# Kernel tuning notes

Measured on AMD Instinct MI355X. Metric: run time of the kernel, lower is better.

## Reference

```python
import jax, jax.numpy as jnp
import numpy as np

N_NODES = 50000


def _degree_norm(src, dst, n):
    # symmetric GCN normalization with self-loops already appended
    deg = jax.ops.segment_sum(jnp.ones(src.shape[0], jnp.float32), dst, num_segments=n)
    dinv = jnp.where(deg > 0, jax.lax.rsqrt(deg), 0.0)
    return dinv[src] * dinv[dst]  # [E_full]


def _gcn_layer(x, W, b, src, dst, norm, n):
    h = x @ W                                  # [N, out]
    msgs = h[src] * norm[:, None]              # gather + scale, [E_full, out]
    out = jax.ops.segment_sum(msgs, dst, num_segments=n)
    return out + b


def setup_inputs() -> dict:
    key = jax.random.key(0)
    k1, k2, k3, k4 = jax.random.split(key, 4)
    n, e, d_in, d_out = N_NODES, 800000, 256, 128
    x = jax.random.normal(k1, (n, d_in), jnp.float32)
    edge_index = jax.random.randint(k2, (2, e), 0, n, dtype=jnp.int64)
    W1 = jax.random.normal(k3, (d_in, 2 * d_out), jnp.float32) / np.sqrt(d_in)
    b1 = jnp.zeros((2 * d_out,), jnp.float32)
    W2 = jax.random.normal(k4, (2 * d_out, d_out), jnp.float32) / np.sqrt(2 * d_out)
    b2 = jnp.zeros((d_out,), jnp.float32)
    return {"x": x, "edge_index": edge_index, "W1": W1, "b1": b1, "W2": W2, "b2": b2}


def reference(x, edge_index, W1, b1, W2, b2):
    n = x.shape[0]
    loops = jnp.arange(n, dtype=edge_index.dtype)
    src = jnp.concatenate([edge_index[0], loops])
    dst = jnp.concatenate([edge_index[1], loops])
    norm = _degree_norm(src, dst, n)
    h = jax.nn.relu(_gcn_layer(x, W1, b1, src, dst, norm, n))
    h = jax.nn.relu(_gcn_layer(h, W2, b2, src, dst, norm, n))
    return h
```

## Files before the change

### kernel.cpp

```cpp
#include <hip/hip_runtime.h>
#include <hip/hip_bf16.h>


typedef __attribute__((ext_vector_type(8))) short bf16x8;
typedef __attribute__((ext_vector_type(8))) unsigned short u16x8;
typedef __attribute__((ext_vector_type(4))) float f32x4;

__device__ inline float bf2f(unsigned short u) {
    return __uint_as_float(((unsigned)u) << 16);
}
__device__ inline unsigned short f2bf(float f) {
    unsigned x = __float_as_uint(f);
    unsigned r = (x + 0x7fffu + ((x >> 16) & 1u)) >> 16;
    return (unsigned short)r;
}

__global__ void degree_kernel(const int* __restrict__ dst, unsigned* __restrict__ deg, int E) {
    int e = blockIdx.x * blockDim.x + threadIdx.x;
    if (e < E) atomicAdd(&deg[dst[e]], 1u);
}

__global__ void dinv_kernel(const unsigned* __restrict__ deg, float* __restrict__ dinv, int N) {
    int i = blockIdx.x * blockDim.x + threadIdx.x;
    if (i < N) dinv[i] = rsqrtf((float)(deg[i] + 1u));
}

#define NBIN 512

__global__ __launch_bounds__(256) void hist_lds_kernel(const unsigned* __restrict__ deg,
                                                       int* __restrict__ hist, int N) {
    __shared__ int lh[NBIN];
    const int t = threadIdx.x;
#pragma unroll
    for (int i = 0; i < NBIN / 256; i++) lh[t + i * 256] = 0;
    __syncthreads();
    int idx = blockIdx.x * 256 + t;
    if (idx < N) {
        int b = (int)deg[idx]; if (b > NBIN - 1) b = NBIN - 1;
        atomicAdd(&lh[NBIN - 1 - b], 1);
    }
    __syncthreads();
#pragma unroll
    for (int i = 0; i < NBIN / 256; i++) {
        int v = lh[t + i * 256];
        if (v) atomicAdd(&hist[t + i * 256], v);
    }
}

__global__ void scan_bins_kernel(const int* __restrict__ hist,
                                 int* __restrict__ binstart,
                                 int* __restrict__ bincur,
                                 int* __restrict__ edgebase,
                                 int* __restrict__ rowptr, int N) {
    const int t = threadIdx.x;
    int cn = 0, ce = 0;
    for (int b = 0; b < NBIN; b += 64) {
        int i = b + t;
        int cnt = hist[i];
        int d = NBIN - 1 - i;
        int d8 = (d + 7) & ~7;
        int en = cnt * d8;
        int xn = cnt, xe = en;
#pragma unroll
        for (int off = 1; off < 64; off <<= 1) {
            int yn = __shfl_up(xn, off, 64);
            int ye = __shfl_up(xe, off, 64);
            if (t >= off) { xn += yn; xe += ye; }
        }
        binstart[i] = cn + xn - cnt;
        bincur[i]   = cn + xn - cnt;
        edgebase[i] = ce + xe - en;
        cn += __shfl(xn, 63, 64);
        ce += __shfl(xe, 63, 64);
    }
    if (t == 0) rowptr[N] = ce;
}

__global__ __launch_bounds__(256) void place_fused_kernel(
    const unsigned* __restrict__ deg,
    int* __restrict__ bincur,
    const int* __restrict__ binstart,
    const int* __restrict__ edgebase,
    int* __restrict__ perm, int* __restrict__ rankv,
    int* __restrict__ rowptr, int* __restrict__ cursor,
    unsigned short* __restrict__ col, int N) {
    __shared__ int lh[NBIN];
    __shared__ int base[NBIN];
    const int t = threadIdx.x;
#pragma unroll
    for (int i = 0; i < NBIN / 256; i++) lh[t + i * 256] = 0;
    __syncthreads();
    int idx = blockIdx.x * 256 + t;
    int bin = 0, lrank = 0;
    if (idx < N) {
        int b = (int)deg[idx]; if (b > NBIN - 1) b = NBIN - 1;
        bin = NBIN - 1 - b;
        lrank = atomicAdd(&lh[bin], 1);
    }
    __syncthreads();
#pragma unroll
    for (int i = 0; i < NBIN / 256; i++) {
        int v = lh[t + i * 256];
        if (v) base[t + i * 256] = atomicAdd(&bincur[t + i * 256], v);
    }
    __syncthreads();
    if (idx < N) {
        int pos = base[bin] + lrank;
        int d = NBIN - 1 - bin;
        int d8 = (d + 7) & ~7;
        int rp = edgebase[bin] + (pos - binstart[bin]) * d8;
        perm[pos] = idx;
        rankv[idx] = pos;
        rowptr[pos] = rp;
        cursor[pos] = rp;
        for (int k = d; k < d8; k++) col[rp + k] = (unsigned short)N;
    }
}

__global__ __launch_bounds__(256) void fill_kernel(const int* __restrict__ src,
                                                   const int* __restrict__ dst,
                                                   const int* __restrict__ rank,
                                                   int* __restrict__ cursor,
                                                   unsigned short* __restrict__ col, int E) {
    int e = blockIdx.x * blockDim.x + threadIdx.x;
    if (e < E) {
        int d = dst[e];
        int pos = atomicAdd(&cursor[rank[d]], 1);
        col[pos] = (unsigned short)src[e];
    }
}

__global__ __launch_bounds__(256) void convert_x_kernel(const float* __restrict__ in,
                                                        const float* __restrict__ dinv,
                                                        unsigned short* __restrict__ out,
                                                        long n4, int ld4) {
    long i = (long)blockIdx.x * blockDim.x + threadIdx.x;
    if (i < n4) {
        float ds = dinv[i / ld4];
        float4 v = ((const float4*)in)[i];
        ushort4 o;
        o.x = f2bf(v.x * ds); o.y = f2bf(v.y * ds);
        o.z = f2bf(v.z * ds); o.w = f2bf(v.w * ds);
        ((ushort4*)out)[i] = o;
    }
}

__global__ __launch_bounds__(256) void convert_wt_kernel(const float* __restrict__ W,
                                                         unsigned short* __restrict__ WT,
                                                         int K, int Nw) {
    int id = blockIdx.x * blockDim.x + threadIdx.x;
    if (id < K * Nw) {
        int k = id / Nw;
        int n = id % Nw;
        WT[(long)n * K + k] = f2bf(W[id]);
    }
}

__global__ void zero_pad_kernel(unsigned short* __restrict__ h1,
                                unsigned short* __restrict__ h2, int Np1) {
    int t = threadIdx.x;
    if (t < 8 * 32) {
        int c = t >> 5, f = t & 31;
        h1[((size_t)c * Np1 + (Np1 - 1)) * 32 + f] = 0;
    } else if (t < 12 * 32) {
        int q = t - 256;
        int c = q >> 5, f = q & 31;
        h2[((size_t)c * Np1 + (Np1 - 1)) * 32 + f] = 0;
    }
}

#define GBM 128
#define GBN 128
#define GBK 64
template <int CH>
__global__ __launch_bounds__(256) void gemm_bf16(const unsigned short* __restrict__ A,
                                                 const unsigned short* __restrict__ BT,
                                                 unsigned short* __restrict__ C,
                                                 int M, int Nc, int K, int ldm) {
    __shared__ __align__(16) unsigned short As[GBM * GBK];
    __shared__ __align__(16) unsigned short Bs[GBN * GBK];
    const int t = threadIdx.x;
    const int lane = t & 63;
    const int w = t >> 6;
    const int row0 = blockIdx.x * GBM;
    const int col0 = blockIdx.y * GBN;
    const int rb = (w >> 1) * 64;
    const int cb = (w & 1) * 64;

    f32x4 acc[4][4] = {};

    for (int kb = 0; kb < K; kb += GBK) {
#pragma unroll
        for (int i = 0; i < 4; i++) {
            int p = i * 256 + t;
            int row = p >> 3;
            int slot = p & 7;
            int chunk = slot ^ (row & 7);
            int grow = row0 + row;
            if (grow >= M) grow = M - 1;
            const unsigned short* src = A + (size_t)grow * K + kb + chunk * 8;
            __builtin_amdgcn_global_load_lds(
                (const __attribute__((address_space(1))) void*)src,
                (__attribute__((address_space(3))) void*)&As[p * 8], 16, 0, 0);
        }
#pragma unroll
        for (int i = 0; i < 4; i++) {
            int p = i * 256 + t;
            int row = p >> 3;
            int slot = p & 7;
            int chunk = slot ^ (row & 7);
            const unsigned short* src = BT + (size_t)(col0 + row) * K + kb + chunk * 8;
            __builtin_amdgcn_global_load_lds(
                (const __attribute__((address_space(1))) void*)src,
                (__attribute__((address_space(3))) void*)&Bs[p * 8], 16, 0, 0);
        }
        asm volatile("s_waitcnt vmcnt(0)" ::: "memory");
        __syncthreads();

#pragma unroll
        for (int ks = 0; ks < 2; ks++) {
            int kq = ks * 4 + (lane >> 4);
            int rsel = lane & 15;
            bf16x8 af[4], bfr[4];
#pragma unroll
            for (int mt = 0; mt < 4; mt++) {
                int m = rb + mt * 16 + rsel;
                int slot = kq ^ (m & 7);
                af[mt] = *(const bf16x8*)&As[m * GBK + slot * 8];
            }
#pragma unroll
            for (int nt = 0; nt < 4; nt++) {
                int n = cb + nt * 16 + rsel;
                int slot = kq ^ (n & 7);
                bfr[nt] = *(const bf16x8*)&Bs[n * GBK + slot * 8];
            }
#pragma unroll
            for (int mt = 0; mt < 4; mt++)
#pragma unroll
                for (int nt = 0; nt < 4; nt++)
                    acc[mt][nt] = __builtin_amdgcn_mfma_f32_16x16x32_bf16(
                        af[mt], bfr[nt], acc[mt][nt], 0, 0, 0);
        }
        __syncthreads();
    }

#pragma unroll
    for (int mt = 0; mt < 4; mt++) {
#pragma unroll
        for (int nt = 0; nt < 4; nt++) {
            int gcol = col0 + cb + nt * 16 + (lane & 15);
            int c = gcol / CH;
            int fo = gcol % CH;
            int grow0 = row0 + rb + mt * 16 + 4 * (lane >> 4);
#pragma unroll
            for (int r = 0; r < 4; r++) {
                int g = grow0 + r;
                if (g < M)
                    C[((size_t)c * ldm + g) * CH + fo] = f2bf(acc[mt][nt][r]);
            }
        }
    }
}

template <int CH, int NCH, bool OUT_BF16>
__global__ __launch_bounds__(512) void gather_cm_kernel(
    const unsigned short* __restrict__ h_cm,
    const int* __restrict__ rowptr,
    const unsigned short* __restrict__ col,
    const int* __restrict__ perm,
    const float* __restrict__ dinv,
    const float* __restrict__ bias,
    void* __restrict__ out,
    int Nn, int F) {
    constexpr int LF = CH / 8;
    constexpr int NS = 64 / LF;
    constexpr int NPB = NS * 8;
    const int chunk = blockIdx.x % NCH;
    const int g = blockIdx.x / NCH;
    const int w = threadIdx.x >> 6;
    const int lane = threadIdx.x & 63;
    const int fl = lane & (LF - 1);
    const int ns = lane / LF;
    const int idx = g * NPB + w * NS + ns;
    const bool valid = idx < Nn;
    const int cidx = valid ? idx : Nn - 1;
    const int node = perm[cidx];

    const unsigned short* hc = h_cm + (size_t)chunk * (Nn + 1) * CH;
    const int beg = rowptr[cidx];
    const int nit = (rowptr[cidx + 1] - beg) >> 3;
    const float ddst = dinv[node];
    const int fo = fl * 8;

    float a0[8] = {}, a1[8] = {};
    const unsigned short* cp = col + beg;
    u16x8 cv = *(const u16x8*)cp;
    for (int it = 0; it < nit; ++it) {
        int s0 = cv[0], s1 = cv[1], s2 = cv[2], s3 = cv[3];
        int s4 = cv[4], s5 = cv[5], s6 = cv[6], s7 = cv[7];
        u16x8 u0 = *(const u16x8*)(hc + s0 * CH + fo);
        u16x8 u1 = *(const u16x8*)(hc + s1 * CH + fo);
        u16x8 u2 = *(const u16x8*)(hc + s2 * CH + fo);
        u16x8 u3 = *(const u16x8*)(hc + s3 * CH + fo);
        u16x8 u4 = *(const u16x8*)(hc + s4 * CH + fo);
        u16x8 u5 = *(const u16x8*)(hc + s5 * CH + fo);
        u16x8 u6 = *(const u16x8*)(hc + s6 * CH + fo);
        u16x8 u7 = *(const u16x8*)(hc + s7 * CH + fo);
        cp += 8;
        cv = *(const u16x8*)cp;
#pragma unroll
        for (int j = 0; j < 8; j++) {
            a0[j] += (bf2f(u0[j]) + bf2f(u1[j])) + (bf2f(u2[j]) + bf2f(u3[j]));
            a1[j] += (bf2f(u4[j]) + bf2f(u5[j])) + (bf2f(u6[j]) + bf2f(u7[j]));
        }
    }

    if (valid) {
        u16x8 us = *(const u16x8*)(hc + node * CH + fo);
        const int f0g = chunk * CH + fo;
        f32x4 bv0 = *(const f32x4*)(bias + f0g);
        f32x4 bv1 = *(const f32x4*)(bias + f0g + 4);
        float v[8];
#pragma unroll
        for (int j = 0; j < 8; j++) {
            float b = (j < 4) ? bv0[j] : bv1[j - 4];
            float s = (a0[j] + a1[j]) + bf2f(us[j]);
            v[j] = fmaxf(fmaf(s, ddst, b), 0.f);
        }
        if (OUT_BF16) {
            u16x8 o;
#pragma unroll
            for (int j = 0; j < 8; j++) o[j] = f2bf(v[j] * ddst);
            *(u16x8*)((unsigned short*)out + (size_t)node * F + f0g) = o;
        } else {
            f32x4 o0, o1;
#pragma unroll
            for (int j = 0; j < 4; j++) { o0[j] = v[j]; o1[j] = v[j + 4]; }
            float* op = (float*)out + (size_t)node * F + f0g;
            *(f32x4*)op = o0;
            *(f32x4*)(op + 4) = o1;
        }
    }
}

extern "C" void kernel_launch(void* const* d_in, const int* in_sizes, int n_in,
                              void* d_out, int out_size, void* d_ws, size_t ws_size,
                              hipStream_t stream) {
    const float* x  = (const float*)d_in[0];
    const int* ei   = (const int*)d_in[1];
    const float* W1 = (const float*)d_in[2];
    const float* b1 = (const float*)d_in[3];
    const float* W2 = (const float*)d_in[4];
    const float* b2 = (const float*)d_in[5];

    const int DIN = 256;
    const int N = in_sizes[0] / DIN;
    const int E = in_sizes[1] / 2;
    const int H = in_sizes[3];
    const int DOUT = in_sizes[5];

    const int* src = ei;
    const int* dst = ei + E;

    char* ws = (char*)d_ws;
    unsigned* deg = (unsigned*)ws;                   ws += (size_t)N * 4;
    float* dinv   = (float*)ws;                      ws += (size_t)N * 4;
    int* rowptr   = (int*)ws;                        ws += (size_t)(N + 4) * 4;
    int* hist     = (int*)ws;                        ws += NBIN * 4;
    int* binstart = (int*)ws;                        ws += NBIN * 4;
    int* bincur   = (int*)ws;                        ws += NBIN * 4;
    int* edgebase = (int*)ws;                        ws += NBIN * 4;
    int* perm     = (int*)ws;                        ws += (size_t)N * 4;
    int* rankv    = (int*)ws;                        ws += (size_t)N * 4;
    int* cursor   = (int*)ws;                        ws += (size_t)N * 4;
    unsigned short* col = (unsigned short*)ws;       ws += (size_t)(E + 8 * N + 64) * 2;
    unsigned short* xb  = (unsigned short*)ws;       ws += (size_t)N * DIN * 2;
    unsigned short* w1t = (unsigned short*)ws;       ws += (size_t)DIN * H * 2;
    unsigned short* w2t = (unsigned short*)ws;       ws += (size_t)H * DOUT * 2;
    unsigned short* h1b = (unsigned short*)ws;       ws += (size_t)(N + 1) * H * 2 + 1024;
    unsigned short* y1b = (unsigned short*)ws;       ws += (size_t)N * H * 2;
    unsigned short* h2b = xb;
    float* outp = (float*)d_out;

    hipMemsetAsync(deg, 0, (size_t)N * 4, stream);
    hipMemsetAsync(hist, 0, (size_t)NBIN * 4, stream);
    degree_kernel<<<(E + 255) / 256, 256, 0, stream>>>(dst, deg, E);
    dinv_kernel<<<(N + 255) / 256, 256, 0, stream>>>(deg, dinv, N);
    hist_lds_kernel<<<(N + 255) / 256, 256, 0, stream>>>(deg, hist, N);
    scan_bins_kernel<<<1, 64, 0, stream>>>(hist, binstart, bincur, edgebase, rowptr, N);
    place_fused_kernel<<<(N + 255) / 256, 256, 0, stream>>>(
        deg, bincur, binstart, edgebase, perm, rankv, rowptr, cursor, col, N);
    fill_kernel<<<(E + 255) / 256, 256, 0, stream>>>(src, dst, rankv, cursor, col, E);

    {
        long n4 = (long)N * DIN / 4;
        convert_x_kernel<<<(int)((n4 + 255) / 256), 256, 0, stream>>>(x, dinv, xb, n4, DIN / 4);
        convert_wt_kernel<<<(DIN * H + 255) / 256, 256, 0, stream>>>(W1, w1t, DIN, H);
        convert_wt_kernel<<<(H * DOUT + 255) / 256, 256, 0, stream>>>(W2, w2t, H, DOUT);
    }

    {
        dim3 grid((N + GBM - 1) / GBM, H / GBN);
        gemm_bf16<32><<<grid, 256, 0, stream>>>(xb, w1t, h1b, N, H, DIN, N + 1);
    }
    zero_pad_kernel<<<1, 384, 0, stream>>>(h1b, h2b, N + 1);
    {
        constexpr int NPB1 = (64 / (32 / 8)) * 8;
        gather_cm_kernel<32, 8, true><<<8 * ((N + NPB1 - 1) / NPB1), 512, 0, stream>>>(
            h1b, rowptr, col, perm, dinv, b1, y1b, N, H);
    }

    {
        dim3 grid((N + GBM - 1) / GBM, DOUT / GBN);
        gemm_bf16<32><<<grid, 256, 0, stream>>>(y1b, w2t, h2b, N, DOUT, H, N + 1);
    }
    {
        constexpr int NPB2 = (64 / (32 / 8)) * 8;
        gather_cm_kernel<32, 4, false><<<4 * ((N + NPB2 - 1) / NPB2), 512, 0, stream>>>(
            h2b, rowptr, col, perm, dinv, b2, outp, N, DOUT);
    }
}
```

Before: 337.7 us.

## Fuse x conversion into first GEMM and merge small preprocessing kernels

The first GEMM now reads fp32 x directly, scales each row by dinv and converts to bf16 while staging into LDS, so the separate x conversion pass and its bf16 buffer are gone. The dinv and histogram kernels are merged, the two weight transposes and the zero-pad kernel are folded into one launch, and the two memsets are combined. Fill now indexes cursor by node id, which drops the rank indirection array. The cost is that the A tile is loaded through registers with fp32 traffic instead of async LDS loads, and x is read twice (once per column block), which could slow the GEMM.

New measurement: 313.5 us. 7.2% less time.

```diff
diff --git a/kernel.cpp b/kernel.cpp
--- a/kernel.cpp
+++ b/kernel.cpp
@@ -15,20 +15,16 @@
     return (unsigned short)r;
 }
 
+#define NBIN 512
+
 __global__ void degree_kernel(const int* __restrict__ dst, unsigned* __restrict__ deg, int E) {
     int e = blockIdx.x * blockDim.x + threadIdx.x;
     if (e < E) atomicAdd(&deg[dst[e]], 1u);
 }
 
-__global__ void dinv_kernel(const unsigned* __restrict__ deg, float* __restrict__ dinv, int N) {
-    int i = blockIdx.x * blockDim.x + threadIdx.x;
-    if (i < N) dinv[i] = rsqrtf((float)(deg[i] + 1u));
-}
-
-#define NBIN 512
-
-__global__ __launch_bounds__(256) void hist_lds_kernel(const unsigned* __restrict__ deg,
-                                                       int* __restrict__ hist, int N) {
+__global__ __launch_bounds__(256) void dinv_hist_kernel(const unsigned* __restrict__ deg,
+                                                        float* __restrict__ dinv,
+                                                        int* __restrict__ hist, int N) {
     __shared__ int lh[NBIN];
     const int t = threadIdx.x;
 #pragma unroll
@@ -36,7 +32,9 @@
     __syncthreads();
     int idx = blockIdx.x * 256 + t;
     if (idx < N) {
-        int b = (int)deg[idx]; if (b > NBIN - 1) b = NBIN - 1;
+        unsigned d = deg[idx];
+        dinv[idx] = rsqrtf((float)(d + 1u));
+        int b = (int)d; if (b > NBIN - 1) b = NBIN - 1;
         atomicAdd(&lh[NBIN - 1 - b], 1);
     }
     __syncthreads();
@@ -81,7 +79,7 @@
     int* __restrict__ bincur,
     const int* __restrict__ binstart,
     const int* __restrict__ edgebase,
-    int* __restrict__ perm, int* __restrict__ rankv,
+    int* __restrict__ perm,
     int* __restrict__ rowptr, int* __restrict__ cursor,
     unsigned short* __restrict__ col, int N) {
     __shared__ int lh[NBIN];
@@ -110,68 +108,149 @@
         int d8 = (d + 7) & ~7;
         int rp = edgebase[bin] + (pos - binstart[bin]) * d8;
         perm[pos] = idx;
-        rankv[idx] = pos;
         rowptr[pos] = rp;
-        cursor[pos] = rp;
+        cursor[idx] = rp;
         for (int k = d; k < d8; k++) col[rp + k] = (unsigned short)N;
     }
 }
 
 __global__ __launch_bounds__(256) void fill_kernel(const int* __restrict__ src,
                                                    const int* __restrict__ dst,
-                                                   const int* __restrict__ rank,
                                                    int* __restrict__ cursor,
                                                    unsigned short* __restrict__ col, int E) {
     int e = blockIdx.x * blockDim.x + threadIdx.x;
     if (e < E) {
         int d = dst[e];
-        int pos = atomicAdd(&cursor[rank[d]], 1);
+        int pos = atomicAdd(&cursor[d], 1);
         col[pos] = (unsigned short)src[e];
     }
 }
 
-__global__ __launch_bounds__(256) void convert_x_kernel(const float* __restrict__ in,
-                                                        const float* __restrict__ dinv,
-                                                        unsigned short* __restrict__ out,
-                                                        long n4, int ld4) {
-    long i = (long)blockIdx.x * blockDim.x + threadIdx.x;
-    if (i < n4) {
-        float ds = dinv[i / ld4];
-        float4 v = ((const float4*)in)[i];
-        ushort4 o;
-        o.x = f2bf(v.x * ds); o.y = f2bf(v.y * ds);
-        o.z = f2bf(v.z * ds); o.w = f2bf(v.w * ds);
-        ((ushort4*)out)[i] = o;
-    }
-}
-
-__global__ __launch_bounds__(256) void convert_wt_kernel(const float* __restrict__ W,
-                                                         unsigned short* __restrict__ WT,
-                                                         int K, int Nw) {
-    int id = blockIdx.x * blockDim.x + threadIdx.x;
-    if (id < K * Nw) {
-        int k = id / Nw;
-        int n = id % Nw;
-        WT[(long)n * K + k] = f2bf(W[id]);
-    }
-}
-
-__global__ void zero_pad_kernel(unsigned short* __restrict__ h1,
-                                unsigned short* __restrict__ h2, int Np1) {
-    int t = threadIdx.x;
-    if (t < 8 * 32) {
-        int c = t >> 5, f = t & 31;
-        h1[((size_t)c * Np1 + (Np1 - 1)) * 32 + f] = 0;
-    } else if (t < 12 * 32) {
-        int q = t - 256;
-        int c = q >> 5, f = q & 31;
-        h2[((size_t)c * Np1 + (Np1 - 1)) * 32 + f] = 0;
+__global__ __launch_bounds__(256) void convwt_pad_kernel(
+    const float* __restrict__ W1, const float* __restrict__ W2,
+    unsigned short* __restrict__ w1t, unsigned short* __restrict__ w2t,
+    unsigned short* __restrict__ h1b, unsigned short* __restrict__ h2b,
+    int DIN, int H, int DOUT, int Np1) {
+    int id = blockIdx.x * 256 + threadIdx.x;
+    int n1 = DIN * H;
+    int n2 = H * DOUT;
+    if (id < n1) {
+        int k = id / H, n = id % H;
+        w1t[(long)n * DIN + k] = f2bf(W1[id]);
+    } else if (id < n1 + n2) {
+        int q = id - n1;
+        int k = q / DOUT, n = q % DOUT;
+        w2t[(long)n * H + k] = f2bf(W2[q]);
+    } else if (id < n1 + n2 + 384) {
+        int q = id - n1 - n2;
+        if (q < 256) {
+            int c = q >> 5, f = q & 31;
+            h1b[((size_t)c * Np1 + (Np1 - 1)) * 32 + f] = 0;
+        } else {
+            int q2 = q - 256;
+            int c = q2 >> 5, f = q2 & 31;
+            h2b[((size_t)c * Np1 + (Np1 - 1)) * 32 + f] = 0;
+        }
     }
 }
 
 #define GBM 128
 #define GBN 128
 #define GBK 64
+__global__ __launch_bounds__(256) void gemm_x_bf16(const float* __restrict__ X,
+                                                   const float* __restrict__ dinv,
+                                                   const unsigned short* __restrict__ BT,
+                                                   unsigned short* __restrict__ C,
+                                                   int M, int Nc, int K, int ldm) {
+    __shared__ __align__(16) unsigned short As[GBM * GBK];
+    __shared__ __align__(16) unsigned short Bs[GBN * GBK];
+    const int t = threadIdx.x;
+    const int lane = t & 63;
+    const int w = t >> 6;
+    const int row0 = blockIdx.x * GBM;
+    const int col0 = blockIdx.y * GBN;
+    const int rb = (w >> 1) * 64;
+    const int cb = (w & 1) * 64;
+
+    f32x4 acc[4][4] = {};
+
+    for (int kb = 0; kb < K; kb += GBK) {
+#pragma unroll
+        for (int i = 0; i < 4; i++) {
+            int p = i * 256 + t;
+            int row = p >> 3;
+            int slot = p & 7;
+            int chunk = slot ^ (row & 7);
+            int grow = row0 + row;
+            if (grow >= M) grow = M - 1;
+            const float* sp = X + (size_t)grow * K + kb + chunk * 8;
+            f32x4 v0 = *(const f32x4*)sp;
+            f32x4 v1 = *(const f32x4*)(sp + 4);
+            float ds = dinv[grow];
+            u16x8 o;
+#pragma unroll
+            for (int j = 0; j < 4; j++) { o[j] = f2bf(v0[j] * ds); o[j + 4] = f2bf(v1[j] * ds); }
+            *(u16x8*)&As[p * 8] = o;
+        }
+#pragma unroll
+        for (int i = 0; i < 4; i++) {
+            int p = i * 256 + t;
+            int row = p >> 3;
+            int slot = p & 7;
+            int chunk = slot ^ (row & 7);
+            const unsigned short* src = BT + (size_t)(col0 + row) * K + kb + chunk * 8;
+            __builtin_amdgcn_global_load_lds(
+                (const __attribute__((address_space(1))) void*)src,
+                (__attribute__((address_space(3))) void*)&Bs[p * 8], 16, 0, 0);
+        }
+        asm volatile("s_waitcnt vmcnt(0)" ::: "memory");
+        __syncthreads();
+
+#pragma unroll
+        for (int ks = 0; ks < 2; ks++) {
+            int kq = ks * 4 + (lane >> 4);
+            int rsel = lane & 15;
+            bf16x8 af[4], bfr[4];
+#pragma unroll
+            for (int mt = 0; mt < 4; mt++) {
+                int m = rb + mt * 16 + rsel;
+                int slot = kq ^ (m & 7);
+                af[mt] = *(const bf16x8*)&As[m * GBK + slot * 8];
+            }
+#pragma unroll
+            for (int nt = 0; nt < 4; nt++) {
+                int n = cb + nt * 16 + rsel;
+                int slot = kq ^ (n & 7);
+                bfr[nt] = *(const bf16x8*)&Bs[n * GBK + slot * 8];
+            }
+#pragma unroll
+            for (int mt = 0; mt < 4; mt++)
+#pragma unroll
+                for (int nt = 0; nt < 4; nt++)
+                    acc[mt][nt] = __builtin_amdgcn_mfma_f32_16x16x32_bf16(
+                        af[mt], bfr[nt], acc[mt][nt], 0, 0, 0);
+        }
+        __syncthreads();
+    }
+
+#pragma unroll
+    for (int mt = 0; mt < 4; mt++) {
+#pragma unroll
+        for (int nt = 0; nt < 4; nt++) {
+            int gcol = col0 + cb + nt * 16 + (lane & 15);
+            int c = gcol >> 5;
+            int fo = gcol & 31;
+            int grow0 = row0 + rb + mt * 16 + 4 * (lane >> 4);
+#pragma unroll
+            for (int r = 0; r < 4; r++) {
+                int g = grow0 + r;
+                if (g < M)
+                    C[((size_t)c * ldm + g) * 32 + fo] = f2bf(acc[mt][nt][r]);
+            }
+        }
+    }
+}
+
 template <int CH>
 __global__ __launch_bounds__(256) void gemm_bf16(const unsigned short* __restrict__ A,
                                                  const unsigned short* __restrict__ BT,
@@ -364,46 +443,40 @@
 
     char* ws = (char*)d_ws;
     unsigned* deg = (unsigned*)ws;                   ws += (size_t)N * 4;
+    int* hist     = (int*)ws;                        ws += NBIN * 4;
     float* dinv   = (float*)ws;                      ws += (size_t)N * 4;
     int* rowptr   = (int*)ws;                        ws += (size_t)(N + 4) * 4;
-    int* hist     = (int*)ws;                        ws += NBIN * 4;
     int* binstart = (int*)ws;                        ws += NBIN * 4;
     int* bincur   = (int*)ws;                        ws += NBIN * 4;
     int* edgebase = (int*)ws;                        ws += NBIN * 4;
     int* perm     = (int*)ws;                        ws += (size_t)N * 4;
-    int* rankv    = (int*)ws;                        ws += (size_t)N * 4;
     int* cursor   = (int*)ws;                        ws += (size_t)N * 4;
     unsigned short* col = (unsigned short*)ws;       ws += (size_t)(E + 8 * N + 64) * 2;
-    unsigned short* xb  = (unsigned short*)ws;       ws += (size_t)N * DIN * 2;
     unsigned short* w1t = (unsigned short*)ws;       ws += (size_t)DIN * H * 2;
     unsigned short* w2t = (unsigned short*)ws;       ws += (size_t)H * DOUT * 2;
     unsigned short* h1b = (unsigned short*)ws;       ws += (size_t)(N + 1) * H * 2 + 1024;
     unsigned short* y1b = (unsigned short*)ws;       ws += (size_t)N * H * 2;
-    unsigned short* h2b = xb;
+    unsigned short* h2b = (unsigned short*)ws;       ws += (size_t)(N + 1) * DOUT * 2 + 1024;
     float* outp = (float*)d_out;
 
-    hipMemsetAsync(deg, 0, (size_t)N * 4, stream);
-    hipMemsetAsync(hist, 0, (size_t)NBIN * 4, stream);
+    hipMemsetAsync(deg, 0, (size_t)N * 4 + NBIN * 4, stream);
     degree_kernel<<<(E + 255) / 256, 256, 0, stream>>>(dst, deg, E);
-    dinv_kernel<<<(N + 255) / 256, 256, 0, stream>>>(deg, dinv, N);
-    hist_lds_kernel<<<(N + 255) / 256, 256, 0, stream>>>(deg, hist, N);
+    dinv_hist_kernel<<<(N + 255) / 256, 256, 0, stream>>>(deg, dinv, hist, N);
     scan_bins_kernel<<<1, 64, 0, stream>>>(hist, binstart, bincur, edgebase, rowptr, N);
     place_fused_kernel<<<(N + 255) / 256, 256, 0, stream>>>(
-        deg, bincur, binstart, edgebase, perm, rankv, rowptr, cursor, col, N);
-    fill_kernel<<<(E + 255) / 256, 256, 0, stream>>>(src, dst, rankv, cursor, col, E);
+        deg, bincur, binstart, edgebase, perm, rowptr, cursor, col, N);
+    fill_kernel<<<(E + 255) / 256, 256, 0, stream>>>(src, dst, cursor, col, E);
 
     {
-        long n4 = (long)N * DIN / 4;
-        convert_x_kernel<<<(int)((n4 + 255) / 256), 256, 0, stream>>>(x, dinv, xb, n4, DIN / 4);
-        convert_wt_kernel<<<(DIN * H + 255) / 256, 256, 0, stream>>>(W1, w1t, DIN, H);
-        convert_wt_kernel<<<(H * DOUT + 255) / 256, 256, 0, stream>>>(W2, w2t, H, DOUT);
+        int tot = DIN * H + H * DOUT + 384;
+        convwt_pad_kernel<<<(tot + 255) / 256, 256, 0, stream>>>(
+            W1, W2, w1t, w2t, h1b, h2b, DIN, H, DOUT, N + 1);
     }
 
     {
         dim3 grid((N + GBM - 1) / GBM, H / GBN);
-        gemm_bf16<32><<<grid, 256, 0, stream>>>(xb, w1t, h1b, N, H, DIN, N + 1);
-    }
-    zero_pad_kernel<<<1, 384, 0, stream>>>(h1b, h2b, N + 1);
+        gemm_x_bf16<<<grid, 256, 0, stream>>>(x, dinv, w1t, h1b, N, H, DIN, N + 1);
+    }
     {
         constexpr int NPB1 = (64 / (32 / 8)) * 8;
         gather_cm_kernel<32, 8, true><<<8 * ((N + NPB1 - 1) / NPB1), 512, 0, stream>>>(
```
